# Optimization experiments

Measured on AMD Instinct MI355X. Metric: run time of the kernel, lower is better.

## Reference

```python
import jax, jax.numpy as jnp
import numpy as np
from jax import lax

# Dimensions (match init_kwargs / input_specs)
S, I, NO = 64, 128, 64      # num_states, num_inputs, num_outputs
K, D = 64, 64               # stack_size, stack_dim
B, T_LEN = 64, 256          # batch of sequences, sequence length
PSTR_THRESH = 0.01          # push/pop gating threshold from original code


def setup_inputs() -> dict:
    key = jax.random.key(0)
    k0, k1, k2, k3, k4, k5 = jax.random.split(key, 6)
    return {
        "input_seq": jax.random.randint(k0, (B, T_LEN), 0, I),
        "T": jax.random.normal(k1, (S, I, D, S), jnp.float32) * 0.1,
        "O": jax.random.normal(k2, (S, I, D, NO), jnp.float32) * 0.1,
        "push_gate": jax.random.normal(k3, (S, I, 1), jnp.float32) * 0.1,
        "pop_gate": jax.random.normal(k4, (S, I, 1), jnp.float32) * 0.1,
        "push_value": jax.random.normal(k5, (S, I, D), jnp.float32) * 0.1,
        "init_logits": jnp.zeros((S,), jnp.float32),
    }


def _run_seq(seq, T, O, push_gate, pop_gate, push_value, init_logits):
    """Process one sequence of int symbols; returns [T_LEN, NO] output probs."""
    state0 = jax.nn.softmax(init_logits)                    # (S,)
    content0 = jnp.zeros((K, D), T.dtype)                   # stack buffer
    pointer0 = jnp.zeros((K,), T.dtype).at[0].set(1.0)      # soft stack pointer

    def step(carry, inp):
        state, content, pointer = carry
        stack_top = pointer @ content                       # (D,) soft read

        # Output: mixture over states of softmax(stack_top @ O[s, inp])
        out_logits = jnp.einsum('d,sdo->so', stack_top, O[:, inp])
        out_prob = state @ jax.nn.softmax(out_logits, axis=-1)  # (NO,)

        # Push/pop strengths: scalars; original uses .item() so they are detached
        push_s = lax.stop_gradient(jax.nn.sigmoid(push_gate[:, inp, 0] @ state))
        pop_s = lax.stop_gradient(jax.nn.sigmoid(pop_gate[:, inp, 0] @ state))
        push_v = jnp.tanh(state @ push_value[:, inp, :])    # (D,) keeps grad

        # Pop (only applied if pop_s > threshold, as in original)
        shifted_down = jnp.concatenate([pointer[1:], jnp.zeros((1,), pointer.dtype)])
        ptr_pop = pop_s * shifted_down + (1.0 - pop_s) * pointer
        pointer = jnp.where(pop_s > PSTR_THRESH, ptr_pop, pointer)

        # Push (only applied if push_s > threshold)
        shifted_up = jnp.concatenate([jnp.zeros((1,), pointer.dtype), pointer[:-1]])
        ptr_push = push_s * shifted_up + (1.0 - push_s) * pointer
        w = ptr_push[:, None]                                # (K,1) write weights
        do_push = push_s > PSTR_THRESH
        pointer = jnp.where(do_push, ptr_push, pointer)
        content = jnp.where(do_push, content * (1.0 - w) + push_v[None, :] * w, content)

        # State transition uses PRE-update stack_top (as in original)
        trans_logits = jnp.einsum('d,sdn->sn', stack_top, T[:, inp])
        new_state = state @ jax.nn.softmax(trans_logits, axis=-1)
        return (new_state, content, pointer), out_prob

    _, outs = lax.scan(step, (state0, content0, pointer0), seq)
    return outs


def reference(input_seq, T, O, push_gate, pop_gate, push_value, init_logits):
    run = lambda seq: _run_seq(seq, T, O, push_gate, pop_gate, push_value, init_logits)
    return jax.vmap(run)(input_seq)  # (B, T_LEN, NO)
```

## Files before the change

### kernel.cpp

```cpp
#include <hip/hip_runtime.h>
#include <math.h>

namespace {
constexpr int cS = 64, cI = 128, cNO = 64, cK = 64, cD = 64, cB = 64, cT = 256;
constexpr float cTH = 0.01f;
constexpr int NTASK = cB * cT;
typedef float vf4 __attribute__((ext_vector_type(4)));

__device__ inline void st_agent(float* p, float v) {
    __hip_atomic_store(p, v, __ATOMIC_RELAXED, __HIP_MEMORY_SCOPE_AGENT);
}
__device__ inline float ld_agent(const float* p) {
    return __hip_atomic_load(p, __ATOMIC_RELAXED, __HIP_MEMORY_SCOPE_AGENT);
}

__global__ __launch_bounds__(256, 1)
void p1_kernel(const int* __restrict__ seq,
               const float* __restrict__ Tm,
               const float* __restrict__ pgate,
               const float* __restrict__ qgate,
               const float* __restrict__ pval,
               const float* __restrict__ initl,
               float* __restrict__ stbuf,
               int* __restrict__ cnt,
               float* __restrict__ gpart)
{
    const int b  = blockIdx.x >> 2;
    const int jw = blockIdx.x & 3;
    const int tid = threadIdx.x;
    const int wave = tid >> 6, lane = tid & 63;
    const int dq = lane >> 4, o4 = lane & 15;

    __shared__ float s_state[cS], s_stack[cD], s_pushv[cD], s_pvpart[cD];
    __shared__ float s_ptr[cK], s_ptr2[cK], s_w[cK];
    __shared__ float s_content[cK][cD];
    __shared__ float s_redA[4][64], s_redB[4][64], s_npart[4][64];
    __shared__ int   s_seq[cT];
    __shared__ float s_push, s_pop;

    if (wave == 0) {
        float v = initl[lane];
        float m = v;
        #pragma unroll
        for (int sh = 1; sh < 64; sh <<= 1) m = fmaxf(m, __shfl_xor(m, sh));
        float e = expf(v - m);
        float s = e;
        #pragma unroll
        for (int sh = 1; sh < 64; sh <<= 1) s += __shfl_xor(s, sh);
        s_state[lane] = e / s;
    } else if (wave == 1) {
        s_ptr[lane] = (lane == 0) ? 1.0f : 0.0f;
    }
    for (int i = tid; i < cK * cD; i += 256) (&s_content[0][0])[i] = 0.f;
    s_seq[tid] = seq[b * cT + tid];
    __syncthreads();

    for (int t = 0; t < cT; ++t) {
        const int inp = s_seq[t];

        {
            float accA = 0.f;
            #pragma unroll
            for (int j = 0; j < 16; ++j) {
                int k = wave * 16 + j;
                accA += s_ptr[k] * s_content[k][lane];
            }
            float accB = 0.f;
            #pragma unroll
            for (int j = 0; j < 4; ++j) {
                int k = jw * 16 + wave * 4 + j;
                accB += s_state[k] * pval[(k * cI + inp) * cD + lane];
            }
            s_redA[wave][lane] = accA;
            s_redB[wave][lane] = accB;
        }
        __syncthreads();

        float* sb = stbuf + (size_t)(b * cT + t) * 128;
        if (wave == 0) {
            float a = s_redA[0][lane] + s_redA[1][lane] + s_redA[2][lane] + s_redA[3][lane];
            s_stack[lane] = a;
            if (jw == 0) { sb[lane] = a; sb[64 + lane] = s_state[lane]; }
        } else if (wave == 1) {
            s_pvpart[lane] = s_redB[0][lane] + s_redB[1][lane] + s_redB[2][lane] + s_redB[3][lane];
        } else if (wave == 2) {
            float v = pgate[lane * cI + inp] * s_state[lane];
            #pragma unroll
            for (int sh = 1; sh < 64; sh <<= 1) v += __shfl_xor(v, sh);
            if (lane == 0) s_push = 1.0f / (1.0f + expf(-v));
        } else if (wave == 3) {
            float v = qgate[lane * cI + inp] * s_state[lane];
            #pragma unroll
            for (int sh = 1; sh < 64; sh <<= 1) v += __shfl_xor(v, sh);
            if (lane == 0) s_pop = 1.0f / (1.0f + expf(-v));
        }
        __syncthreads();

        {
            float xs[16];
            #pragma unroll
            for (int i = 0; i < 16; ++i) xs[i] = s_stack[dq * 16 + i];

            float4 nacc = make_float4(0.f, 0.f, 0.f, 0.f);
            #pragma unroll
            for (int rp = 0; rp < 2; ++rp) {
                const int sA = jw * 16 + wave * 4 + rp * 2;
                const int sB = sA + 1;
                const float4* rpA =
                    reinterpret_cast<const float4*>(Tm + (size_t)(sA * cI + inp) * (cD * cS)) + o4;
                const float4* rpB =
                    reinterpret_cast<const float4*>(Tm + (size_t)(sB * cI + inp) * (cD * cS)) + o4;
                float4 va[16], vb[16];
                #pragma unroll
                for (int i = 0; i < 16; ++i) {
                    va[i] = rpA[(dq * 16 + i) * 16];
                    vb[i] = rpB[(dq * 16 + i) * 16];
                }
                float4 aA = make_float4(0.f,0.f,0.f,0.f), aB = make_float4(0.f,0.f,0.f,0.f);
                #pragma unroll
                for (int i = 0; i < 16; ++i) {
                    float x = xs[i];
                    aA.x = fmaf(x, va[i].x, aA.x); aA.y = fmaf(x, va[i].y, aA.y);
                    aA.z = fmaf(x, va[i].z, aA.z); aA.w = fmaf(x, va[i].w, aA.w);
                    aB.x = fmaf(x, vb[i].x, aB.x); aB.y = fmaf(x, vb[i].y, aB.y);
                    aB.z = fmaf(x, vb[i].z, aB.z); aB.w = fmaf(x, vb[i].w, aB.w);
                }
                #pragma unroll
                for (int m = 16; m < 64; m <<= 1) {
                    aA.x += __shfl_xor(aA.x, m); aA.y += __shfl_xor(aA.y, m);
                    aA.z += __shfl_xor(aA.z, m); aA.w += __shfl_xor(aA.w, m);
                    aB.x += __shfl_xor(aB.x, m); aB.y += __shfl_xor(aB.y, m);
                    aB.z += __shfl_xor(aB.z, m); aB.w += __shfl_xor(aB.w, m);
                }
                float mA = fmaxf(fmaxf(aA.x, aA.y), fmaxf(aA.z, aA.w));
                float mB = fmaxf(fmaxf(aB.x, aB.y), fmaxf(aB.z, aB.w));
                #pragma unroll
                for (int m = 1; m < 16; m <<= 1) {
                    mA = fmaxf(mA, __shfl_xor(mA, m));
                    mB = fmaxf(mB, __shfl_xor(mB, m));
                }
                float4 eA, eB;
                eA.x = expf(aA.x - mA); eA.y = expf(aA.y - mA);
                eA.z = expf(aA.z - mA); eA.w = expf(aA.w - mA);
                eB.x = expf(aB.x - mB); eB.y = expf(aB.y - mB);
                eB.z = expf(aB.z - mB); eB.w = expf(aB.w - mB);
                float smA = eA.x + eA.y + eA.z + eA.w;
                float smB = eB.x + eB.y + eB.z + eB.w;
                #pragma unroll
                for (int m = 1; m < 16; m <<= 1) {
                    smA += __shfl_xor(smA, m);
                    smB += __shfl_xor(smB, m);
                }
                float cA = s_state[sA] / smA;
                float cB = s_state[sB] / smB;
                nacc.x = fmaf(cA, eA.x, nacc.x); nacc.x = fmaf(cB, eB.x, nacc.x);
                nacc.y = fmaf(cA, eA.y, nacc.y); nacc.y = fmaf(cB, eB.y, nacc.y);
                nacc.z = fmaf(cA, eA.z, nacc.z); nacc.z = fmaf(cB, eB.z, nacc.z);
                nacc.w = fmaf(cA, eA.w, nacc.w); nacc.w = fmaf(cB, eB.w, nacc.w);
            }
            if (dq == 0) {
                s_npart[wave][o4 * 4 + 0] = nacc.x;
                s_npart[wave][o4 * 4 + 1] = nacc.y;
                s_npart[wave][o4 * 4 + 2] = nacc.z;
                s_npart[wave][o4 * 4 + 3] = nacc.w;
            }
        }
        __syncthreads();

        float* gq = gpart + ((size_t)(b * 2 + (t & 1)) * 4 + jw) * 128;
        if (wave == 0) {
            float np = s_npart[0][lane] + s_npart[1][lane] + s_npart[2][lane] + s_npart[3][lane];
            st_agent(gq + lane, np);
            st_agent(gq + 64 + lane, s_pvpart[lane]);
            asm volatile("s_waitcnt vmcnt(0)" ::: "memory");
            if (lane == 0)
                __hip_atomic_fetch_add(cnt + b * cT + t, 1, __ATOMIC_RELAXED, __HIP_MEMORY_SCOPE_AGENT);
        } else if (wave == 1) {
            float p  = s_ptr[lane];
            float sd = (lane < cK - 1) ? s_ptr[lane + 1] : 0.f;
            float pop = s_pop;
            float pp = pop * sd + (1.f - pop) * p;
            s_ptr2[lane] = (pop > cTH) ? pp : p;
        }
        __syncthreads();

        if (tid == 0) {
            int* c = cnt + b * cT + t;
            while (__hip_atomic_load(c, __ATOMIC_RELAXED, __HIP_MEMORY_SCOPE_AGENT) < 4) {}
        }
        __syncthreads();

        const float* gb = gpart + (size_t)(b * 2 + (t & 1)) * 4 * 128;
        if (wave == 0) {
            float ns = 0.f;
            #pragma unroll
            for (int q = 0; q < 4; ++q) ns += ld_agent(gb + q * 128 + lane);
            s_state[lane] = ns;
        } else if (wave == 1) {
            float pv = 0.f;
            #pragma unroll
            for (int q = 0; q < 4; ++q) pv += ld_agent(gb + q * 128 + 64 + lane);
            s_pushv[lane] = tanhf(pv);
        }
        __syncthreads();

        if (wave == 0) {
            float p2 = s_ptr2[lane];
            float su = (lane > 0) ? s_ptr2[lane - 1] : 0.f;
            float push = s_push;
            float pp = push * su + (1.f - push) * p2;
            s_w[lane] = pp;
            s_ptr[lane] = (push > cTH) ? pp : p2;
        }
        __syncthreads();

        if (s_push > cTH) {
            for (int idx = tid; idx < cK * cD; idx += 256) {
                int k = idx >> 6, d = idx & 63;
                float w = s_w[k];
                s_content[k][d] = s_content[k][d] * (1.f - w) + s_pushv[d] * w;
            }
        }
        __syncthreads();
    }
}

__global__ void k_count(const int* __restrict__ seq, int* __restrict__ counts) {
    int i = blockIdx.x * 256 + threadIdx.x;
    if (i < NTASK) atomicAdd(&counts[seq[i]], 1);
}
__global__ void k_scan(const int* __restrict__ counts, int* __restrict__ offsets,
                       int* __restrict__ cursor) {
    const int lane = threadIdx.x & 63;
    int c0 = counts[lane], c1 = counts[64 + lane];
    int s0 = c0, s1 = c1;
    #pragma unroll
    for (int m = 1; m < 64; m <<= 1) {
        int t0 = __shfl_up(s0, m);
        int t1 = __shfl_up(s1, m);
        if (lane >= m) { s0 += t0; s1 += t1; }
    }
    int tot0 = __shfl(s0, 63);
    int e0 = s0 - c0;
    int e1 = tot0 + s1 - c1;
    offsets[lane] = e0;       cursor[lane] = e0;
    offsets[64 + lane] = e1;  cursor[64 + lane] = e1;
    if (lane == 63) offsets[128] = tot0 + __shfl(s1, 63);
}
__global__ void k_scatter(const int* __restrict__ seq, int* __restrict__ cursor,
                          int* __restrict__ tasks) {
    int i = blockIdx.x * 256 + threadIdx.x;
    if (i < NTASK) {
        int pos = atomicAdd(&cursor[seq[i]], 1);
        tasks[pos] = i;
    }
}

__global__ __launch_bounds__(512, 2)
void p2_kernel(const float* __restrict__ Om,
               const float* __restrict__ stbuf,
               const int* __restrict__ offsets,
               const int* __restrict__ tasks,
               float* __restrict__ out)
{
    const int g = blockIdx.x >> 1, h = blockIdx.x & 1;
    const int tid = threadIdx.x, wave = tid >> 6, lane = tid & 63;
    const int dq = lane >> 4, o4 = lane & 15;

    const int beg = offsets[g], end = offsets[g + 1];
    const int n = end - beg, half = (n + 1) >> 1;
    const int hbeg = beg + h * half;
    const int hend = h ? end : (beg + half);
    const int cnt = hend - hbeg;
    if (cnt <= 0) return;
    const int nsweep = (cnt + 63) >> 6;

    __shared__ vf4 sO[2][1024];

    const vf4* O0 = reinterpret_cast<const vf4*>(Om) + (size_t)g * 1024;
    const size_t rowstride = (size_t)cI * 1024;

    for (int sweep = 0; sweep < nsweep; ++sweep) {
        int   tsk[8];
        bool  val[8];
        float stv[8][16];
        float sstate[8];
        vf4   acc[8];
        #pragma unroll
        for (int u = 0; u < 8; ++u) {
            int idx = hbeg + sweep * 64 + (u >> 2) * 32 + wave * 4 + (u & 3);
            bool v = idx < hend;
            val[u] = v;
            int id = tasks[v ? idx : hbeg];
            id = __builtin_amdgcn_readfirstlane(id);
            tsk[u] = id;
            const float* sp = stbuf + (size_t)id * 128;
            #pragma unroll
            for (int i = 0; i < 16; ++i) stv[u][i] = sp[dq * 16 + i];
            sstate[u] = sp[64 + lane];
            acc[u].x = 0.f; acc[u].y = 0.f; acc[u].z = 0.f; acc[u].w = 0.f;
        }

        vf4 r0 = __builtin_nontemporal_load(O0 + (size_t)tid * 2);
        vf4 r1 = __builtin_nontemporal_load(O0 + (size_t)tid * 2 + 1);

        for (int s = 0; s < cS; ++s) {
            sO[s & 1][tid * 2]     = r0;
            sO[s & 1][tid * 2 + 1] = r1;
            __syncthreads();
            if (s + 1 < cS) {
                const vf4* nr = O0 + (size_t)(s + 1) * rowstride;
                r0 = __builtin_nontemporal_load(nr + (size_t)tid * 2);
                r1 = __builtin_nontemporal_load(nr + (size_t)tid * 2 + 1);
            }
            vf4 part[8];
            #pragma unroll
            for (int u = 0; u < 8; ++u) { part[u].x = 0.f; part[u].y = 0.f; part[u].z = 0.f; part[u].w = 0.f; }
            #pragma unroll
            for (int i = 0; i < 16; ++i) {
                vf4 ovi = sO[s & 1][(dq * 16 + i) * 16 + o4];
                #pragma unroll
                for (int u = 0; u < 8; ++u) {
                    float x = stv[u][i];
                    part[u].x = fmaf(x, ovi.x, part[u].x);
                    part[u].y = fmaf(x, ovi.y, part[u].y);
                    part[u].z = fmaf(x, ovi.z, part[u].z);
                    part[u].w = fmaf(x, ovi.w, part[u].w);
                }
            }
            #pragma unroll
            for (int u = 0; u < 8; ++u) {
                vf4 a = part[u];
                #pragma unroll
                for (int m = 16; m < 64; m <<= 1) {
                    a.x += __shfl_xor(a.x, m); a.y += __shfl_xor(a.y, m);
                    a.z += __shfl_xor(a.z, m); a.w += __shfl_xor(a.w, m);
                }
                float mx = fmaxf(fmaxf(a.x, a.y), fmaxf(a.z, a.w));
                #pragma unroll
                for (int m = 1; m < 16; m <<= 1) mx = fmaxf(mx, __shfl_xor(mx, m));
                vf4 e;
                e.x = expf(a.x - mx); e.y = expf(a.y - mx);
                e.z = expf(a.z - mx); e.w = expf(a.w - mx);
                float sm = e.x + e.y + e.z + e.w;
                #pragma unroll
                for (int m = 1; m < 16; m <<= 1) sm += __shfl_xor(sm, m);
                float coef = __shfl(sstate[u], s) / sm;
                acc[u].x = fmaf(coef, e.x, acc[u].x);
                acc[u].y = fmaf(coef, e.y, acc[u].y);
                acc[u].z = fmaf(coef, e.z, acc[u].z);
                acc[u].w = fmaf(coef, e.w, acc[u].w);
            }
        }
        #pragma unroll
        for (int u = 0; u < 8; ++u) {
            if (val[u] && dq == 0) {
                float* op = out + (size_t)tsk[u] * cNO + o4 * 4;
                op[0] = acc[u].x; op[1] = acc[u].y; op[2] = acc[u].z; op[3] = acc[u].w;
            }
        }
    }
}

__global__ __launch_bounds__(512, 1)
void fpt_mono(const int* __restrict__ seq, const float* __restrict__ Tm,
              const float* __restrict__ Om, const float* __restrict__ pgate,
              const float* __restrict__ qgate, const float* __restrict__ pval,
              const float* __restrict__ initl, float* __restrict__ out)
{
    const int b = blockIdx.x;
    const int tid = threadIdx.x;
    const int wave = tid >> 6, lane = tid & 63;
    const int dq = lane >> 4, o4 = lane & 15;

    __shared__ float s_state[cS], s_nstate[cS], s_stack[cD], s_pushv[cD];
    __shared__ float s_ptr[cK], s_ptr2[cK], s_w[cK];
    __shared__ float s_content[cK][cD];
    __shared__ float s_redA[8][64], s_redB[8][64];
    __shared__ float s_opart[4][cNO], s_npart[4][cS];
    __shared__ float s_push, s_pop;

    if (wave == 0) {
        float v = initl[lane];
        float m = v;
        #pragma unroll
        for (int sh = 1; sh < 64; sh <<= 1) m = fmaxf(m, __shfl_xor(m, sh));
        float e = expf(v - m);
        float s = e;
        #pragma unroll
        for (int sh = 1; sh < 64; sh <<= 1) s += __shfl_xor(s, sh);
        s_state[lane] = e / s;
    } else if (wave == 1) s_ptr[lane] = (lane == 0) ? 1.0f : 0.0f;
    for (int idx = tid; idx < cK * cD; idx += 512) (&s_content[0][0])[idx] = 0.0f;
    __syncthreads();

    for (int t = 0; t < cT; ++t) {
        const int inp = seq[b * cT + t];
        {
            float accA = 0.f, accB = 0.f;
            #pragma unroll
            for (int j = 0; j < 8; ++j) {
                int k = wave * 8 + j;
                accA += s_ptr[k] * s_content[k][lane];
                accB += s_state[k] * pval[(k * cI + inp) * cD + lane];
            }
            s_redA[wave][lane] = accA;
            s_redB[wave][lane] = accB;
        }
        __syncthreads();
        if (wave == 0) {
            float a = 0.f;
            #pragma unroll
            for (int g = 0; g < 8; ++g) a += s_redA[g][lane];
            s_stack[lane] = a;
        } else if (wave == 1) {
            float a = 0.f;
            #pragma unroll
            for (int g = 0; g < 8; ++g) a += s_redB[g][lane];
            s_pushv[lane] = tanhf(a);
        } else if (wave == 2) {
            float v = pgate[lane * cI + inp] * s_state[lane];
            #pragma unroll
            for (int sh = 1; sh < 64; sh <<= 1) v += __shfl_xor(v, sh);
            if (lane == 0) s_push = 1.0f / (1.0f + expf(-v));
        } else if (wave == 3) {
            float v = qgate[lane * cI + inp] * s_state[lane];
            #pragma unroll
            for (int sh = 1; sh < 64; sh <<= 1) v += __shfl_xor(v, sh);
            if (lane == 0) s_pop = 1.0f / (1.0f + expf(-v));
        }
        __syncthreads();
        {
            const bool isO = (wave < 4);
            const int w4 = wave & 3;
            const float* Mbase = isO ? Om : Tm;
            float xs[16];
            #pragma unroll
            for (int i = 0; i < 16; ++i) xs[i] = s_stack[dq * 16 + i];
            float4 oacc = make_float4(0.f, 0.f, 0.f, 0.f);
            for (int r = 0; r < 16; ++r) {
                const int s = w4 * 16 + r;
                const float4* rowp =
                    reinterpret_cast<const float4*>(Mbase + (size_t)(s * cI + inp) * (cD * 64)) + o4;
                float4 acc = make_float4(0.f, 0.f, 0.f, 0.f);
                #pragma unroll
                for (int i = 0; i < 16; ++i) {
                    float4 mv = rowp[(dq * 16 + i) * 16];
                    float xd = xs[i];
                    acc.x = fmaf(xd, mv.x, acc.x); acc.y = fmaf(xd, mv.y, acc.y);
                    acc.z = fmaf(xd, mv.z, acc.z); acc.w = fmaf(xd, mv.w, acc.w);
                }
                #pragma unroll
                for (int m = 16; m < 64; m <<= 1) {
                    acc.x += __shfl_xor(acc.x, m); acc.y += __shfl_xor(acc.y, m);
                    acc.z += __shfl_xor(acc.z, m); acc.w += __shfl_xor(acc.w, m);
                }
                float mx = fmaxf(fmaxf(acc.x, acc.y), fmaxf(acc.z, acc.w));
                #pragma unroll
                for (int m = 1; m < 16; m <<= 1) mx = fmaxf(mx, __shfl_xor(mx, m));
                float4 e;
                e.x = expf(acc.x - mx); e.y = expf(acc.y - mx);
                e.z = expf(acc.z - mx); e.w = expf(acc.w - mx);
                float sm = e.x + e.y + e.z + e.w;
                #pragma unroll
                for (int m = 1; m < 16; m <<= 1) sm += __shfl_xor(sm, m);
                float coef = s_state[s] / sm;
                oacc.x = fmaf(coef, e.x, oacc.x); oacc.y = fmaf(coef, e.y, oacc.y);
                oacc.z = fmaf(coef, e.z, oacc.z); oacc.w = fmaf(coef, e.w, oacc.w);
            }
            if (dq == 0) {
                float* dst = isO ? &s_opart[w4][0] : &s_npart[w4][0];
                dst[o4 * 4 + 0] = oacc.x; dst[o4 * 4 + 1] = oacc.y;
                dst[o4 * 4 + 2] = oacc.z; dst[o4 * 4 + 3] = oacc.w;
            }
        }
        __syncthreads();
        if (wave == 0) {
            float o = s_opart[0][lane] + s_opart[1][lane] + s_opart[2][lane] + s_opart[3][lane];
            out[((size_t)b * cT + t) * cNO + lane] = o;
        } else if (wave == 1) {
            s_nstate[lane] = s_npart[0][lane] + s_npart[1][lane] + s_npart[2][lane] + s_npart[3][lane];
        } else if (wave == 2) {
            float p = s_ptr[lane];
            float sd = (lane < cK - 1) ? s_ptr[lane + 1] : 0.f;
            float pop = s_pop;
            float pp = pop * sd + (1.f - pop) * p;
            s_ptr2[lane] = (pop > cTH) ? pp : p;
        }
        __syncthreads();
        if (wave == 0) {
            float p2 = s_ptr2[lane];
            float su = (lane > 0) ? s_ptr2[lane - 1] : 0.f;
            float push = s_push;
            float pp = push * su + (1.f - push) * p2;
            s_w[lane] = pp;
            s_ptr[lane] = (push > cTH) ? pp : p2;
        } else if (wave == 1) {
            s_state[lane] = s_nstate[lane];
        }
        __syncthreads();
        if (s_push > cTH) {
            for (int idx = tid; idx < cK * cD; idx += 512) {
                int k = idx >> 6, d = idx & 63;
                float w = s_w[k];
                s_content[k][d] = s_content[k][d] * (1.f - w) + s_pushv[d] * w;
            }
        }
        __syncthreads();
    }
}
}

extern "C" void kernel_launch(void* const* d_in, const int* in_sizes, int n_in,
                              void* d_out, int out_size, void* d_ws, size_t ws_size,
                              hipStream_t stream) {
    const int*   seq = (const int*)d_in[0];
    const float* Tm  = (const float*)d_in[1];
    const float* Om  = (const float*)d_in[2];
    const float* pg  = (const float*)d_in[3];
    const float* qg  = (const float*)d_in[4];
    const float* pv  = (const float*)d_in[5];
    const float* il  = (const float*)d_in[6];
    float* o = (float*)d_out;

    const size_t stbuf_bytes  = (size_t)NTASK * 128 * sizeof(float);
    const size_t counts_off   = stbuf_bytes;
    const size_t offsets_off  = counts_off + 128 * sizeof(int);
    const size_t cursor_off   = offsets_off + 132 * sizeof(int);
    const size_t tasks_off    = cursor_off + 128 * sizeof(int);
    const size_t cnt_off      = tasks_off + (size_t)NTASK * sizeof(int);
    const size_t gpart_off    = cnt_off + (size_t)NTASK * sizeof(int);
    const size_t need         = gpart_off + (size_t)cB * 2 * 4 * 128 * sizeof(float);

    if (ws_size < need) {
        hipLaunchKernelGGL(fpt_mono, dim3(cB), dim3(512), 0, stream,
                           seq, Tm, Om, pg, qg, pv, il, o);
        return;
    }

    float* stbuf  = (float*)d_ws;
    int* counts   = (int*)((char*)d_ws + counts_off);
    int* offsets  = (int*)((char*)d_ws + offsets_off);
    int* cursor   = (int*)((char*)d_ws + cursor_off);
    int* tasks    = (int*)((char*)d_ws + tasks_off);
    int* cnt      = (int*)((char*)d_ws + cnt_off);
    float* gpart  = (float*)((char*)d_ws + gpart_off);

    hipMemsetAsync(counts, 0, 128 * sizeof(int), stream);
    hipMemsetAsync(cnt, 0, (size_t)NTASK * sizeof(int), stream);
    hipLaunchKernelGGL(k_count,   dim3(NTASK / 256), dim3(256), 0, stream, seq, counts);
    hipLaunchKernelGGL(k_scan,    dim3(1),           dim3(64),  0, stream, counts, offsets, cursor);
    hipLaunchKernelGGL(k_scatter, dim3(NTASK / 256), dim3(256), 0, stream, seq, cursor, tasks);
    hipLaunchKernelGGL(p1_kernel, dim3(cB * 4), dim3(256), 0, stream,
                       seq, Tm, pg, qg, pv, il, stbuf, cnt, gpart);
    hipLaunchKernelGGL(p2_kernel, dim3(256), dim3(512), 0, stream, Om, stbuf, offsets, tasks, o);
}
```

Before: 3.039 ms.

## Prefetch next-step weights into registers and merge cross-block sync phases

Each step's T, push_value and gate loads are now issued one timestep ahead into a register buffer, so the serial recurrence no longer waits on global memory latency. Wave 0 handles the inter-block spin-wait and reduction alone, and the pop/push pointer update is fused into a single wave using a shuffle. This removes two block barriers per step. The plain syncthreads are replaced with raw LDS-only barriers. In exchange, register pressure rises (64 vf4 per thread) and correctness relies on the hand-placed waitcnt/barrier ordering.

```diff
diff --git a/kernel.cpp b/kernel.cpp
--- a/kernel.cpp
+++ b/kernel.cpp
@@ -13,6 +13,9 @@
 __device__ inline float ld_agent(const float* p) {
     return __hip_atomic_load(p, __ATOMIC_RELAXED, __HIP_MEMORY_SCOPE_AGENT);
 }
+
+#define BARLDS() do { asm volatile("s_waitcnt lgkmcnt(0)" ::: "memory"); \
+                      __builtin_amdgcn_s_barrier(); } while (0)
 
 __global__ __launch_bounds__(256, 1)
 void p1_kernel(const int* __restrict__ seq,
@@ -30,9 +33,10 @@
     const int tid = threadIdx.x;
     const int wave = tid >> 6, lane = tid & 63;
     const int dq = lane >> 4, o4 = lane & 15;
+    const int baseS = jw * 16 + wave * 4;
 
     __shared__ float s_state[cS], s_stack[cD], s_pushv[cD], s_pvpart[cD];
-    __shared__ float s_ptr[cK], s_ptr2[cK], s_w[cK];
+    __shared__ float s_ptr[cK], s_w[cK];
     __shared__ float s_content[cK][cD];
     __shared__ float s_redA[4][64], s_redB[4][64], s_npart[4][64];
     __shared__ int   s_seq[cT];
@@ -55,8 +59,28 @@
     s_seq[tid] = seq[b * cT + tid];
     __syncthreads();
 
+    vf4  tv[4][16];
+    float pv4[4], pgv, qgv;
+
+    auto PREFETCH = [&](int ip) {
+        #pragma unroll
+        for (int r = 0; r < 4; ++r) {
+            const vf4* rp = reinterpret_cast<const vf4*>(
+                Tm + (size_t)((baseS + r) * cI + ip) * (cD * cS)) + o4;
+            #pragma unroll
+            for (int i = 0; i < 16; ++i) tv[r][i] = rp[(dq * 16 + i) * 16];
+        }
+        #pragma unroll
+        for (int j = 0; j < 4; ++j)
+            pv4[j] = pval[((size_t)(baseS + j) * cI + ip) * cD + lane];
+        pgv = pgate[lane * cI + ip];
+        qgv = qgate[lane * cI + ip];
+    };
+
+    PREFETCH(s_seq[0]);
+
     for (int t = 0; t < cT; ++t) {
-        const int inp = s_seq[t];
+        const int ipn = s_seq[(t + 1 < cT) ? t + 1 : cT - 1];
 
         {
             float accA = 0.f;
@@ -67,14 +91,11 @@
             }
             float accB = 0.f;
             #pragma unroll
-            for (int j = 0; j < 4; ++j) {
-                int k = jw * 16 + wave * 4 + j;
-                accB += s_state[k] * pval[(k * cI + inp) * cD + lane];
-            }
+            for (int j = 0; j < 4; ++j) accB += s_state[baseS + j] * pv4[j];
             s_redA[wave][lane] = accA;
             s_redB[wave][lane] = accB;
         }
-        __syncthreads();
+        BARLDS();
 
         float* sb = stbuf + (size_t)(b * cT + t) * 128;
         if (wave == 0) {
@@ -84,17 +105,17 @@
         } else if (wave == 1) {
             s_pvpart[lane] = s_redB[0][lane] + s_redB[1][lane] + s_redB[2][lane] + s_redB[3][lane];
         } else if (wave == 2) {
-            float v = pgate[lane * cI + inp] * s_state[lane];
+            float v = pgv * s_state[lane];
             #pragma unroll
             for (int sh = 1; sh < 64; sh <<= 1) v += __shfl_xor(v, sh);
             if (lane == 0) s_push = 1.0f / (1.0f + expf(-v));
-        } else if (wave == 3) {
-            float v = qgate[lane * cI + inp] * s_state[lane];
+        } else {
+            float v = qgv * s_state[lane];
             #pragma unroll
             for (int sh = 1; sh < 64; sh <<= 1) v += __shfl_xor(v, sh);
             if (lane == 0) s_pop = 1.0f / (1.0f + expf(-v));
         }
-        __syncthreads();
+        BARLDS();
 
         {
             float xs[16];
@@ -103,60 +124,35 @@
 
             float4 nacc = make_float4(0.f, 0.f, 0.f, 0.f);
             #pragma unroll
-            for (int rp = 0; rp < 2; ++rp) {
-                const int sA = jw * 16 + wave * 4 + rp * 2;
-                const int sB = sA + 1;
-                const float4* rpA =
-                    reinterpret_cast<const float4*>(Tm + (size_t)(sA * cI + inp) * (cD * cS)) + o4;
-                const float4* rpB =
-                    reinterpret_cast<const float4*>(Tm + (size_t)(sB * cI + inp) * (cD * cS)) + o4;
-                float4 va[16], vb[16];
-                #pragma unroll
-                for (int i = 0; i < 16; ++i) {
-                    va[i] = rpA[(dq * 16 + i) * 16];
-                    vb[i] = rpB[(dq * 16 + i) * 16];
-                }
-                float4 aA = make_float4(0.f,0.f,0.f,0.f), aB = make_float4(0.f,0.f,0.f,0.f);
+            for (int r = 0; r < 4; ++r) {
+                vf4 a; a.x = 0.f; a.y = 0.f; a.z = 0.f; a.w = 0.f;
                 #pragma unroll
                 for (int i = 0; i < 16; ++i) {
                     float x = xs[i];
-                    aA.x = fmaf(x, va[i].x, aA.x); aA.y = fmaf(x, va[i].y, aA.y);
-                    aA.z = fmaf(x, va[i].z, aA.z); aA.w = fmaf(x, va[i].w, aA.w);
-                    aB.x = fmaf(x, vb[i].x, aB.x); aB.y = fmaf(x, vb[i].y, aB.y);
-                    aB.z = fmaf(x, vb[i].z, aB.z); aB.w = fmaf(x, vb[i].w, aB.w);
+                    a.x = fmaf(x, tv[r][i].x, a.x);
+                    a.y = fmaf(x, tv[r][i].y, a.y);
+                    a.z = fmaf(x, tv[r][i].z, a.z);
+                    a.w = fmaf(x, tv[r][i].w, a.w);
                 }
                 #pragma unroll
                 for (int m = 16; m < 64; m <<= 1) {
-                    aA.x += __shfl_xor(aA.x, m); aA.y += __shfl_xor(aA.y, m);
-                    aA.z += __shfl_xor(aA.z, m); aA.w += __shfl_xor(aA.w, m);
-                    aB.x += __shfl_xor(aB.x, m); aB.y += __shfl_xor(aB.y, m);
-                    aB.z += __shfl_xor(aB.z, m); aB.w += __shfl_xor(aB.w, m);
+                    a.x += __shfl_xor(a.x, m); a.y += __shfl_xor(a.y, m);
+                    a.z += __shfl_xor(a.z, m); a.w += __shfl_xor(a.w, m);
                 }
-                float mA = fmaxf(fmaxf(aA.x, aA.y), fmaxf(aA.z, aA.w));
-                float mB = fmaxf(fmaxf(aB.x, aB.y), fmaxf(aB.z, aB.w));
-                #pragma unroll
-                for (int m = 1; m < 16; m <<= 1) {
-                    mA = fmaxf(mA, __shfl_xor(mA, m));
-                    mB = fmaxf(mB, __shfl_xor(mB, m));
-                }
-                float4 eA, eB;
-                eA.x = expf(aA.x - mA); eA.y = expf(aA.y - mA);
-                eA.z = expf(aA.z - mA); eA.w = expf(aA.w - mA);
-                eB.x = expf(aB.x - mB); eB.y = expf(aB.y - mB);
-                eB.z = expf(aB.z - mB); eB.w = expf(aB.w - mB);
-                float smA = eA.x + eA.y + eA.z + eA.w;
-                float smB = eB.x + eB.y + eB.z + eB.w;
-                #pragma unroll
-                for (int m = 1; m < 16; m <<= 1) {
-                    smA += __shfl_xor(smA, m);
-                    smB += __shfl_xor(smB, m);
-                }
-                float cA = s_state[sA] / smA;
-                float cB = s_state[sB] / smB;
-                nacc.x = fmaf(cA, eA.x, nacc.x); nacc.x = fmaf(cB, eB.x, nacc.x);
-                nacc.y = fmaf(cA, eA.y, nacc.y); nacc.y = fmaf(cB, eB.y, nacc.y);
-                nacc.z = fmaf(cA, eA.z, nacc.z); nacc.z = fmaf(cB, eB.z, nacc.z);
-                nacc.w = fmaf(cA, eA.w, nacc.w); nacc.w = fmaf(cB, eB.w, nacc.w);
+                float mx = fmaxf(fmaxf(a.x, a.y), fmaxf(a.z, a.w));
+                #pragma unroll
+                for (int m = 1; m < 16; m <<= 1) mx = fmaxf(mx, __shfl_xor(mx, m));
+                vf4 e;
+                e.x = expf(a.x - mx); e.y = expf(a.y - mx);
+                e.z = expf(a.z - mx); e.w = expf(a.w - mx);
+                float sm = e.x + e.y + e.z + e.w;
+                #pragma unroll
+                for (int m = 1; m < 16; m <<= 1) sm += __shfl_xor(sm, m);
+                float coef = s_state[baseS + r] / sm;
+                nacc.x = fmaf(coef, e.x, nacc.x);
+                nacc.y = fmaf(coef, e.y, nacc.y);
+                nacc.z = fmaf(coef, e.z, nacc.z);
+                nacc.w = fmaf(coef, e.w, nacc.w);
             }
             if (dq == 0) {
                 s_npart[wave][o4 * 4 + 0] = nacc.x;
@@ -165,63 +161,55 @@
                 s_npart[wave][o4 * 4 + 3] = nacc.w;
             }
         }
-        __syncthreads();
-
-        float* gq = gpart + ((size_t)(b * 2 + (t & 1)) * 4 + jw) * 128;
+        if (wave != 0) PREFETCH(ipn);
+        BARLDS();
+
         if (wave == 0) {
+            float* gq = gpart + ((size_t)(b * 2 + (t & 1)) * 4 + jw) * 128;
             float np = s_npart[0][lane] + s_npart[1][lane] + s_npart[2][lane] + s_npart[3][lane];
             st_agent(gq + lane, np);
             st_agent(gq + 64 + lane, s_pvpart[lane]);
             asm volatile("s_waitcnt vmcnt(0)" ::: "memory");
+            int* c = cnt + b * cT + t;
             if (lane == 0)
-                __hip_atomic_fetch_add(cnt + b * cT + t, 1, __ATOMIC_RELAXED, __HIP_MEMORY_SCOPE_AGENT);
+                __hip_atomic_fetch_add(c, 1, __ATOMIC_RELAXED, __HIP_MEMORY_SCOPE_AGENT);
+            while (__hip_atomic_load(c, __ATOMIC_RELAXED, __HIP_MEMORY_SCOPE_AGENT) < 4) {}
+            const float* gb = gpart + (size_t)(b * 2 + (t & 1)) * 4 * 128;
+            float ns = 0.f, pvs = 0.f;
+            #pragma unroll
+            for (int q = 0; q < 4; ++q) {
+                ns  += ld_agent(gb + q * 128 + lane);
+                pvs += ld_agent(gb + q * 128 + 64 + lane);
+            }
+            s_state[lane] = ns;
+            s_pushv[lane] = tanhf(pvs);
+            __builtin_amdgcn_sched_barrier(0);
+            PREFETCH(ipn);
         } else if (wave == 1) {
             float p  = s_ptr[lane];
             float sd = (lane < cK - 1) ? s_ptr[lane + 1] : 0.f;
             float pop = s_pop;
-            float pp = pop * sd + (1.f - pop) * p;
-            s_ptr2[lane] = (pop > cTH) ? pp : p;
-        }
-        __syncthreads();
-
-        if (tid == 0) {
-            int* c = cnt + b * cT + t;
-            while (__hip_atomic_load(c, __ATOMIC_RELAXED, __HIP_MEMORY_SCOPE_AGENT) < 4) {}
-        }
-        __syncthreads();
-
-        const float* gb = gpart + (size_t)(b * 2 + (t & 1)) * 4 * 128;
-        if (wave == 0) {
-            float ns = 0.f;
-            #pragma unroll
-            for (int q = 0; q < 4; ++q) ns += ld_agent(gb + q * 128 + lane);
-            s_state[lane] = ns;
-        } else if (wave == 1) {
-            float pv = 0.f;
-            #pragma unroll
-            for (int q = 0; q < 4; ++q) pv += ld_agent(gb + q * 128 + 64 + lane);
-            s_pushv[lane] = tanhf(pv);
-        }
-        __syncthreads();
-
-        if (wave == 0) {
-            float p2 = s_ptr2[lane];
-            float su = (lane > 0) ? s_ptr2[lane - 1] : 0.f;
+            float ppo = pop * sd + (1.f - pop) * p;
+            float p2  = (pop > cTH) ? ppo : p;
+            float su  = __shfl_up(p2, 1);
+            if (lane == 0) su = 0.f;
             float push = s_push;
-            float pp = push * su + (1.f - push) * p2;
-            s_w[lane] = pp;
-            s_ptr[lane] = (push > cTH) ? pp : p2;
-        }
-        __syncthreads();
+            float ppu = push * su + (1.f - push) * p2;
+            s_w[lane] = ppu;
+            s_ptr[lane] = (push > cTH) ? ppu : p2;
+        }
+        BARLDS();
 
         if (s_push > cTH) {
-            for (int idx = tid; idx < cK * cD; idx += 256) {
+            #pragma unroll
+            for (int it = 0; it < 16; ++it) {
+                int idx = tid + it * 256;
                 int k = idx >> 6, d = idx & 63;
                 float w = s_w[k];
                 s_content[k][d] = s_content[k][d] * (1.f - w) + s_pushv[d] * w;
             }
         }
-        __syncthreads();
+        BARLDS();
     }
 }
 
```

Result: slower. 3.315 ms (+9.1%).

## Double p1 block size and merge barrier phases in recurrent step

Applied to the files above, without the earlier changes.

Raises the p1 recurrence kernel to 512 threads, so each wave handles two transition-matrix states instead of four and half as many pointer rows and push-value rows. The cross-block spin-wait, global partial sums and pointer update are folded into one phase: wave 0 waits and reduces while wave 1 computes pop and push pointer updates with a lane shuffle. This drops two __syncthreads per time step and shortens each wave's serial critical path. In exchange there are more waves per block and 8-way LDS reductions.

```diff
diff --git a/kernel.cpp b/kernel.cpp
--- a/kernel.cpp
+++ b/kernel.cpp
@@ -14,7 +14,7 @@
     return __hip_atomic_load(p, __ATOMIC_RELAXED, __HIP_MEMORY_SCOPE_AGENT);
 }
 
-__global__ __launch_bounds__(256, 1)
+__global__ __launch_bounds__(512, 1)
 void p1_kernel(const int* __restrict__ seq,
                const float* __restrict__ Tm,
                const float* __restrict__ pgate,
@@ -32,9 +32,9 @@
     const int dq = lane >> 4, o4 = lane & 15;
 
     __shared__ float s_state[cS], s_stack[cD], s_pushv[cD], s_pvpart[cD];
-    __shared__ float s_ptr[cK], s_ptr2[cK], s_w[cK];
+    __shared__ float s_ptr[cK], s_w[cK];
     __shared__ float s_content[cK][cD];
-    __shared__ float s_redA[4][64], s_redB[4][64], s_npart[4][64];
+    __shared__ float s_redA[8][64], s_redB[8][64], s_npart[8][64];
     __shared__ int   s_seq[cT];
     __shared__ float s_push, s_pop;
 
@@ -51,8 +51,8 @@
     } else if (wave == 1) {
         s_ptr[lane] = (lane == 0) ? 1.0f : 0.0f;
     }
-    for (int i = tid; i < cK * cD; i += 256) (&s_content[0][0])[i] = 0.f;
-    s_seq[tid] = seq[b * cT + tid];
+    for (int i = tid; i < cK * cD; i += 512) (&s_content[0][0])[i] = 0.f;
+    if (tid < cT) s_seq[tid] = seq[b * cT + tid];
     __syncthreads();
 
     for (int t = 0; t < cT; ++t) {
@@ -61,15 +61,15 @@
         {
             float accA = 0.f;
             #pragma unroll
-            for (int j = 0; j < 16; ++j) {
-                int k = wave * 16 + j;
+            for (int j = 0; j < 8; ++j) {
+                int k = wave * 8 + j;
                 accA += s_ptr[k] * s_content[k][lane];
             }
             float accB = 0.f;
             #pragma unroll
-            for (int j = 0; j < 4; ++j) {
-                int k = jw * 16 + wave * 4 + j;
-                accB += s_state[k] * pval[(k * cI + inp) * cD + lane];
+            for (int j = 0; j < 2; ++j) {
+                int k = jw * 16 + wave * 2 + j;
+                accB += s_state[k] * pval[((size_t)k * cI + inp) * cD + lane];
             }
             s_redA[wave][lane] = accA;
             s_redB[wave][lane] = accB;
@@ -78,11 +78,16 @@
 
         float* sb = stbuf + (size_t)(b * cT + t) * 128;
         if (wave == 0) {
-            float a = s_redA[0][lane] + s_redA[1][lane] + s_redA[2][lane] + s_redA[3][lane];
+            float a = 0.f;
+            #pragma unroll
+            for (int g = 0; g < 8; ++g) a += s_redA[g][lane];
             s_stack[lane] = a;
-            if (jw == 0) { sb[lane] = a; sb[64 + lane] = s_state[lane]; }
+            if (jw == 0) sb[lane] = a;
         } else if (wave == 1) {
-            s_pvpart[lane] = s_redB[0][lane] + s_redB[1][lane] + s_redB[2][lane] + s_redB[3][lane];
+            float a = 0.f;
+            #pragma unroll
+            for (int g = 0; g < 8; ++g) a += s_redB[g][lane];
+            s_pvpart[lane] = a;
         } else if (wave == 2) {
             float v = pgate[lane * cI + inp] * s_state[lane];
             #pragma unroll
@@ -93,6 +98,8 @@
             #pragma unroll
             for (int sh = 1; sh < 64; sh <<= 1) v += __shfl_xor(v, sh);
             if (lane == 0) s_pop = 1.0f / (1.0f + expf(-v));
+        } else if (wave == 4) {
+            if (jw == 0) sb[64 + lane] = s_state[lane];
         }
         __syncthreads();
 
@@ -101,63 +108,62 @@
             #pragma unroll
             for (int i = 0; i < 16; ++i) xs[i] = s_stack[dq * 16 + i];
 
-            float4 nacc = make_float4(0.f, 0.f, 0.f, 0.f);
-            #pragma unroll
-            for (int rp = 0; rp < 2; ++rp) {
-                const int sA = jw * 16 + wave * 4 + rp * 2;
-                const int sB = sA + 1;
-                const float4* rpA =
-                    reinterpret_cast<const float4*>(Tm + (size_t)(sA * cI + inp) * (cD * cS)) + o4;
-                const float4* rpB =
-                    reinterpret_cast<const float4*>(Tm + (size_t)(sB * cI + inp) * (cD * cS)) + o4;
-                float4 va[16], vb[16];
-                #pragma unroll
-                for (int i = 0; i < 16; ++i) {
-                    va[i] = rpA[(dq * 16 + i) * 16];
-                    vb[i] = rpB[(dq * 16 + i) * 16];
-                }
-                float4 aA = make_float4(0.f,0.f,0.f,0.f), aB = make_float4(0.f,0.f,0.f,0.f);
-                #pragma unroll
-                for (int i = 0; i < 16; ++i) {
-                    float x = xs[i];
-                    aA.x = fmaf(x, va[i].x, aA.x); aA.y = fmaf(x, va[i].y, aA.y);
-                    aA.z = fmaf(x, va[i].z, aA.z); aA.w = fmaf(x, va[i].w, aA.w);
-                    aB.x = fmaf(x, vb[i].x, aB.x); aB.y = fmaf(x, vb[i].y, aB.y);
-                    aB.z = fmaf(x, vb[i].z, aB.z); aB.w = fmaf(x, vb[i].w, aB.w);
-                }
-                #pragma unroll
-                for (int m = 16; m < 64; m <<= 1) {
-                    aA.x += __shfl_xor(aA.x, m); aA.y += __shfl_xor(aA.y, m);
-                    aA.z += __shfl_xor(aA.z, m); aA.w += __shfl_xor(aA.w, m);
-                    aB.x += __shfl_xor(aB.x, m); aB.y += __shfl_xor(aB.y, m);
-                    aB.z += __shfl_xor(aB.z, m); aB.w += __shfl_xor(aB.w, m);
-                }
-                float mA = fmaxf(fmaxf(aA.x, aA.y), fmaxf(aA.z, aA.w));
-                float mB = fmaxf(fmaxf(aB.x, aB.y), fmaxf(aB.z, aB.w));
-                #pragma unroll
-                for (int m = 1; m < 16; m <<= 1) {
-                    mA = fmaxf(mA, __shfl_xor(mA, m));
-                    mB = fmaxf(mB, __shfl_xor(mB, m));
-                }
-                float4 eA, eB;
-                eA.x = expf(aA.x - mA); eA.y = expf(aA.y - mA);
-                eA.z = expf(aA.z - mA); eA.w = expf(aA.w - mA);
-                eB.x = expf(aB.x - mB); eB.y = expf(aB.y - mB);
-                eB.z = expf(aB.z - mB); eB.w = expf(aB.w - mB);
-                float smA = eA.x + eA.y + eA.z + eA.w;
-                float smB = eB.x + eB.y + eB.z + eB.w;
-                #pragma unroll
-                for (int m = 1; m < 16; m <<= 1) {
-                    smA += __shfl_xor(smA, m);
-                    smB += __shfl_xor(smB, m);
-                }
-                float cA = s_state[sA] / smA;
-                float cB = s_state[sB] / smB;
-                nacc.x = fmaf(cA, eA.x, nacc.x); nacc.x = fmaf(cB, eB.x, nacc.x);
-                nacc.y = fmaf(cA, eA.y, nacc.y); nacc.y = fmaf(cB, eB.y, nacc.y);
-                nacc.z = fmaf(cA, eA.z, nacc.z); nacc.z = fmaf(cB, eB.z, nacc.z);
-                nacc.w = fmaf(cA, eA.w, nacc.w); nacc.w = fmaf(cB, eB.w, nacc.w);
-            }
+            const int sA = jw * 16 + wave * 2;
+            const int sB = sA + 1;
+            const vf4* rpA = reinterpret_cast<const vf4*>(
+                Tm + (size_t)(sA * cI + inp) * (cD * cS)) + o4;
+            const vf4* rpB = reinterpret_cast<const vf4*>(
+                Tm + (size_t)(sB * cI + inp) * (cD * cS)) + o4;
+            vf4 va[16], vb[16];
+            #pragma unroll
+            for (int i = 0; i < 16; ++i) {
+                va[i] = rpA[(dq * 16 + i) * 16];
+                vb[i] = rpB[(dq * 16 + i) * 16];
+            }
+            vf4 aA, aB;
+            aA.x = 0.f; aA.y = 0.f; aA.z = 0.f; aA.w = 0.f;
+            aB.x = 0.f; aB.y = 0.f; aB.z = 0.f; aB.w = 0.f;
+            #pragma unroll
+            for (int i = 0; i < 16; ++i) {
+                float x = xs[i];
+                aA.x = fmaf(x, va[i].x, aA.x); aA.y = fmaf(x, va[i].y, aA.y);
+                aA.z = fmaf(x, va[i].z, aA.z); aA.w = fmaf(x, va[i].w, aA.w);
+                aB.x = fmaf(x, vb[i].x, aB.x); aB.y = fmaf(x, vb[i].y, aB.y);
+                aB.z = fmaf(x, vb[i].z, aB.z); aB.w = fmaf(x, vb[i].w, aB.w);
+            }
+            #pragma unroll
+            for (int m = 16; m < 64; m <<= 1) {
+                aA.x += __shfl_xor(aA.x, m); aA.y += __shfl_xor(aA.y, m);
+                aA.z += __shfl_xor(aA.z, m); aA.w += __shfl_xor(aA.w, m);
+                aB.x += __shfl_xor(aB.x, m); aB.y += __shfl_xor(aB.y, m);
+                aB.z += __shfl_xor(aB.z, m); aB.w += __shfl_xor(aB.w, m);
+            }
+            float mA = fmaxf(fmaxf(aA.x, aA.y), fmaxf(aA.z, aA.w));
+            float mB = fmaxf(fmaxf(aB.x, aB.y), fmaxf(aB.z, aB.w));
+            #pragma unroll
+            for (int m = 1; m < 16; m <<= 1) {
+                mA = fmaxf(mA, __shfl_xor(mA, m));
+                mB = fmaxf(mB, __shfl_xor(mB, m));
+            }
+            vf4 eA, eB;
+            eA.x = expf(aA.x - mA); eA.y = expf(aA.y - mA);
+            eA.z = expf(aA.z - mA); eA.w = expf(aA.w - mA);
+            eB.x = expf(aB.x - mB); eB.y = expf(aB.y - mB);
+            eB.z = expf(aB.z - mB); eB.w = expf(aB.w - mB);
+            float smA = eA.x + eA.y + eA.z + eA.w;
+            float smB = eB.x + eB.y + eB.z + eB.w;
+            #pragma unroll
+            for (int m = 1; m < 16; m <<= 1) {
+                smA += __shfl_xor(smA, m);
+                smB += __shfl_xor(smB, m);
+            }
+            float cA = s_state[sA] / smA;
+            float cB = s_state[sB] / smB;
+            vf4 nacc;
+            nacc.x = cA * eA.x + cB * eB.x;
+            nacc.y = cA * eA.y + cB * eB.y;
+            nacc.z = cA * eA.z + cB * eB.z;
+            nacc.w = cA * eA.w + cB * eB.w;
             if (dq == 0) {
                 s_npart[wave][o4 * 4 + 0] = nacc.x;
                 s_npart[wave][o4 * 4 + 1] = nacc.y;
@@ -167,55 +173,46 @@
         }
         __syncthreads();
 
-        float* gq = gpart + ((size_t)(b * 2 + (t & 1)) * 4 + jw) * 128;
         if (wave == 0) {
-            float np = s_npart[0][lane] + s_npart[1][lane] + s_npart[2][lane] + s_npart[3][lane];
+            float* gq = gpart + ((size_t)(b * 2 + (t & 1)) * 4 + jw) * 128;
+            float np = 0.f;
+            #pragma unroll
+            for (int w = 0; w < 8; ++w) np += s_npart[w][lane];
             st_agent(gq + lane, np);
             st_agent(gq + 64 + lane, s_pvpart[lane]);
             asm volatile("s_waitcnt vmcnt(0)" ::: "memory");
+            int* c = cnt + b * cT + t;
             if (lane == 0)
-                __hip_atomic_fetch_add(cnt + b * cT + t, 1, __ATOMIC_RELAXED, __HIP_MEMORY_SCOPE_AGENT);
+                __hip_atomic_fetch_add(c, 1, __ATOMIC_RELAXED, __HIP_MEMORY_SCOPE_AGENT);
+            while (__hip_atomic_load(c, __ATOMIC_RELAXED, __HIP_MEMORY_SCOPE_AGENT) < 4) {}
+            const float* gb = gpart + (size_t)(b * 2 + (t & 1)) * 4 * 128;
+            float ns = 0.f, pvs = 0.f;
+            #pragma unroll
+            for (int q = 0; q < 4; ++q) {
+                ns  += ld_agent(gb + q * 128 + lane);
+                pvs += ld_agent(gb + q * 128 + 64 + lane);
+            }
+            s_state[lane] = ns;
+            s_pushv[lane] = tanhf(pvs);
         } else if (wave == 1) {
             float p  = s_ptr[lane];
             float sd = (lane < cK - 1) ? s_ptr[lane + 1] : 0.f;
             float pop = s_pop;
-            float pp = pop * sd + (1.f - pop) * p;
-            s_ptr2[lane] = (pop > cTH) ? pp : p;
-        }
-        __syncthreads();
-
-        if (tid == 0) {
-            int* c = cnt + b * cT + t;
-            while (__hip_atomic_load(c, __ATOMIC_RELAXED, __HIP_MEMORY_SCOPE_AGENT) < 4) {}
-        }
-        __syncthreads();
-
-        const float* gb = gpart + (size_t)(b * 2 + (t & 1)) * 4 * 128;
-        if (wave == 0) {
-            float ns = 0.f;
-            #pragma unroll
-            for (int q = 0; q < 4; ++q) ns += ld_agent(gb + q * 128 + lane);
-            s_state[lane] = ns;
-        } else if (wave == 1) {
-            float pv = 0.f;
-            #pragma unroll
-            for (int q = 0; q < 4; ++q) pv += ld_agent(gb + q * 128 + 64 + lane);
-            s_pushv[lane] = tanhf(pv);
-        }
-        __syncthreads();
-
-        if (wave == 0) {
-            float p2 = s_ptr2[lane];
-            float su = (lane > 0) ? s_ptr2[lane - 1] : 0.f;
+            float ppo = pop * sd + (1.f - pop) * p;
+            float p2  = (pop > cTH) ? ppo : p;
+            float su  = __shfl_up(p2, 1);
+            if (lane == 0) su = 0.f;
             float push = s_push;
-            float pp = push * su + (1.f - push) * p2;
-            s_w[lane] = pp;
-            s_ptr[lane] = (push > cTH) ? pp : p2;
+            float ppu = push * su + (1.f - push) * p2;
+            s_w[lane] = ppu;
+            s_ptr[lane] = (push > cTH) ? ppu : p2;
         }
         __syncthreads();
 
         if (s_push > cTH) {
-            for (int idx = tid; idx < cK * cD; idx += 256) {
+            #pragma unroll
+            for (int it = 0; it < 8; ++it) {
+                int idx = tid + it * 512;
                 int k = idx >> 6, d = idx & 63;
                 float w = s_w[k];
                 s_content[k][d] = s_content[k][d] * (1.f - w) + s_pushv[d] * w;
@@ -551,7 +548,7 @@
     hipLaunchKernelGGL(k_count,   dim3(NTASK / 256), dim3(256), 0, stream, seq, counts);
     hipLaunchKernelGGL(k_scan,    dim3(1),           dim3(64),  0, stream, counts, offsets, cursor);
     hipLaunchKernelGGL(k_scatter, dim3(NTASK / 256), dim3(256), 0, stream, seq, cursor, tasks);
-    hipLaunchKernelGGL(p1_kernel, dim3(cB * 4), dim3(256), 0, stream,
+    hipLaunchKernelGGL(p1_kernel, dim3(cB * 4), dim3(512), 0, stream,
                        seq, Tm, pg, qg, pv, il, stbuf, cnt, gpart);
     hipLaunchKernelGGL(p2_kernel, dim3(256), dim3(512), 0, stream, Om, stbuf, offsets, tasks, o);
 }
```

After: 2.969 ms. 1.02x faster.
